# Optimization experiments

Measured on AMD Instinct MI355X. Metric: run time of the kernel, lower is better.

Reference implementation:

```python
import jax, jax.numpy as jnp
import numpy as np

IN_F, OUT_F, BLOCK, NBLK = 1024, 4096, 256, 16
TOPK = NBLK // 4  # 4, as in forward: n_blocks // 4


def setup_inputs() -> dict:
    key = jax.random.key(0)
    ks = jax.random.split(key, 7)
    s = 1.0 / np.sqrt(IN_F)
    s2 = 1.0 / np.sqrt(OUT_F)
    return {
        "x": jax.random.normal(ks[0], (4, 4096, IN_F), jnp.float32),
        "router_w": jax.random.uniform(ks[1], (NBLK, IN_F), jnp.float32, -s, s),
        "router_b": jax.random.uniform(ks[2], (NBLK,), jnp.float32, -s, s),
        "w1": jax.random.uniform(ks[3], (OUT_F, IN_F), jnp.float32, -s, s),
        "b1": jax.random.uniform(ks[4], (OUT_F,), jnp.float32, -s, s),
        "w2": jax.random.uniform(ks[5], (IN_F, OUT_F), jnp.float32, -s2, s2),
        "b2": jax.random.uniform(ks[6], (IN_F,), jnp.float32, -s2, s2),
    }


def reference(x, router_w, router_b, w1, b1, w2, b2):
    x_shape = x.shape
    xf = x.reshape(-1, IN_F)  # [N, d]
    n = xf.shape[0]
    # router: Linear + softmax, then top-k block selection per token
    prob = jax.nn.softmax(xf @ router_w.T + router_b, axis=-1)  # [N, n_blocks]
    _, idx = jax.lax.top_k(prob, TOPK)  # [N, k]
    mask = jnp.zeros((n, NBLK), bool).at[jnp.arange(n)[:, None], idx].set(True)
    # RoutedLinearRow: per-block fc1, zeros at unselected blocks
    w1b = w1.reshape(NBLK, BLOCK, IN_F)
    b1b = b1.reshape(NBLK, BLOCK)
    h = jnp.einsum('nd,ibd->nib', xf, w1b) + b1b  # [N, n_blocks, block]
    h = jnp.where(mask[:, :, None], h, jnp.zeros((), h.dtype))
    h = jax.nn.relu(h)
    # RoutedLinearCol: only selected blocks contribute
    w2b = w2.reshape(IN_F, NBLK, BLOCK)
    y = jnp.einsum('nib,dib->nd', jnp.where(mask[:, :, None], h, 0.0), w2b) + b2
    return y.reshape(x_shape)
```

## Files before the change

### kernel.cpp

```cpp
#include <hip/hip_runtime.h>
#include <hip/hip_bf16.h>

#define NTOK   16384
#define INF    1024
#define OUTF   4096
#define NBLK   16
#define BLKSZ  256
#define KTOP   4

typedef short bf16x8 __attribute__((ext_vector_type(8)));
typedef float f32x4 __attribute__((ext_vector_type(4)));
typedef unsigned short u16x8 __attribute__((ext_vector_type(8)));

__device__ __forceinline__ unsigned short f2bf(float f) {
  unsigned u = __float_as_uint(f);
  u += 0x7FFFu + ((u >> 16) & 1u);
  return (unsigned short)(u >> 16);
}

__device__ __forceinline__ void load_lds16(const void* g, void* l) {
  __builtin_amdgcn_global_load_lds(
      (const __attribute__((address_space(1))) unsigned int*)g,
      (__attribute__((address_space(3))) unsigned int*)l, 16, 0, 0);
}

__device__ __forceinline__ double shfl_xor_d(double v, int m) {
  long long l = __double_as_longlong(v);
  int lo = (int)(l & 0xFFFFFFFFll), hi = (int)(l >> 32);
  lo = __shfl_xor(lo, m);
  hi = __shfl_xor(hi, m);
  return __longlong_as_double(((long long)hi << 32) | (unsigned long long)(unsigned)lo);
}

__device__ __forceinline__ int pi_perm(int j) {
  return (j & 128) | ((j & 7) << 4) | ((j >> 3) & 15);
}

__global__ void k_zero(unsigned* __restrict__ list32, unsigned* __restrict__ counts) {
  int i = blockIdx.x * 256 + threadIdx.x;
  if (i < 33792) list32[i] = 0;
  else if (i < 33808) counts[i - 33792] = 0;
}

__global__ __launch_bounds__(256) void k_convert(
    const float* __restrict__ w1, const float* __restrict__ w2,
    const float* __restrict__ b1, unsigned short* __restrict__ w1b,
    unsigned short* __restrict__ w2p, float* __restrict__ b1p) {
  const size_t stride = (size_t)gridDim.x * 256;
  for (size_t i = (size_t)blockIdx.x * 256 + threadIdx.x; i < 1573376; i += stride) {
    if (i < 1048576) {
      float4 v = ((const float4*)w1)[i];
      ushort4 o;
      o.x = f2bf(v.x); o.y = f2bf(v.y); o.z = f2bf(v.z); o.w = f2bf(v.w);
      ((ushort4*)w1b)[i] = o;
    } else if (i < 1572864) {
      const size_t g = i - 1048576;
      const int d = (int)(g >> 9);
      const int rest = (int)(g & 511);
      const int jg = rest * 8;
      const int blk = jg >> 8;
      const int j0 = jg & 255;
      const float* src = w2 + (size_t)d * 4096 + blk * 256;
      u16x8 o;
#pragma unroll
      for (int ni = 0; ni < 8; ++ni) o[ni] = f2bf(src[pi_perm(j0 + ni)]);
      *(u16x8*)(w2p + (size_t)d * 4096 + jg) = o;
    } else {
      const int idx = (int)(i - 1572864);
      const int jg = idx * 8;
      const int blk = jg >> 8;
      const int j0 = jg & 255;
      const float* src = b1 + blk * 256;
      float o[8];
#pragma unroll
      for (int ni = 0; ni < 8; ++ni) o[ni] = src[pi_perm(j0 + ni)];
      float4* dst = (float4*)(b1p + jg);
      dst[0] = make_float4(o[0], o[1], o[2], o[3]);
      dst[1] = make_float4(o[4], o[5], o[6], o[7]);
    }
  }
}

__global__ __launch_bounds__(256) void k_router(
    const float* __restrict__ x, const float* __restrict__ rw,
    const float* __restrict__ rb, unsigned* __restrict__ tok_blocks,
    unsigned* __restrict__ counts, unsigned short* __restrict__ xb) {
  __shared__ float4 rwl[4096];
  const int tid = threadIdx.x;
  const float4* rw4 = (const float4*)rw;
  for (int i = tid; i < 4096; i += 256) rwl[i] = rw4[i];
  __syncthreads();

  const int n = blockIdx.x * 32 + (tid >> 3);
  const int q = tid & 7;
  double p[16];
#pragma unroll
  for (int j = 0; j < 16; ++j) p[j] = 0.0;
  const float4* xr = (const float4*)(x + (size_t)n * INF);
  ushort4* xbr = (ushort4*)(xb + (size_t)n * INF);
#pragma unroll 4
  for (int i = 0; i < 32; ++i) {
    const int d4 = q + i * 8;
    const float4 xv = xr[d4];
    ushort4 o;
    o.x = f2bf(xv.x); o.y = f2bf(xv.y); o.z = f2bf(xv.z); o.w = f2bf(xv.w);
    xbr[d4] = o;
#pragma unroll
    for (int j = 0; j < 16; ++j) {
      const float4 wv = rwl[j * 256 + d4];
      p[j] = fma((double)xv.x, (double)wv.x, p[j]);
      p[j] = fma((double)xv.y, (double)wv.y, p[j]);
      p[j] = fma((double)xv.z, (double)wv.z, p[j]);
      p[j] = fma((double)xv.w, (double)wv.w, p[j]);
    }
  }
#pragma unroll
  for (int j = 0; j < 16; ++j) {
    double v = p[j];
    v += shfl_xor_d(v, 1);
    v += shfl_xor_d(v, 2);
    v += shfl_xor_d(v, 4);
    p[j] = v + (double)rb[j];
  }

  __syncthreads();
  unsigned* hist = (unsigned*)rwl;
  if (tid < 16) hist[tid] = 0;
  __syncthreads();

  if (q == 0) {
    unsigned packed = 0;
#pragma unroll
    for (int j = 0; j < 16; ++j) {
      int r = 0;
#pragma unroll
      for (int j2 = 0; j2 < 16; ++j2)
        r += (int)((p[j2] > p[j]) | ((p[j2] == p[j]) & (j2 < j)));
      if (r < KTOP) packed |= (unsigned)j << (8 * r);
    }
    tok_blocks[n] = packed;
    atomicAdd(&hist[packed & 15u], 1u);
    atomicAdd(&hist[(packed >> 8) & 15u], 1u);
    atomicAdd(&hist[(packed >> 16) & 15u], 1u);
    atomicAdd(&hist[(packed >> 24) & 15u], 1u);
  }
  __syncthreads();
  if (tid < 16 && hist[tid]) atomicAdd(&counts[tid], hist[tid]);
}

__global__ void k_scan(const unsigned* __restrict__ counts, unsigned* __restrict__ off,
                       unsigned* __restrict__ cursors) {
  if (threadIdx.x == 0 && blockIdx.x == 0) {
    unsigned o = 0;
    for (int i = 0; i < 16; ++i) {
      off[i] = o; cursors[i] = o;
      o += (counts[i] + 127u) & ~127u;
    }
    off[16] = o;
  }
}

__global__ __launch_bounds__(256) void k_build(
    const unsigned* __restrict__ tok_blocks, unsigned* __restrict__ cursors,
    unsigned short* __restrict__ list, unsigned* __restrict__ inv) {
  const int n = blockIdx.x * 256 + threadIdx.x;
  const unsigned packed = tok_blocks[n];
  const int lane = threadIdx.x & 63;
  for (int b = 0; b < 16; ++b) {
    int r = -1;
#pragma unroll
    for (int q = 0; q < 4; ++q)
      if (((packed >> (8 * q)) & 15u) == (unsigned)b) r = q;
    unsigned long long m = __ballot(r >= 0);
    if (m) {
      int leader = __ffsll((unsigned long long)m) - 1;
      unsigned base = 0;
      if (lane == leader) base = atomicAdd(&cursors[b], (unsigned)__popcll(m));
      base = (unsigned)__shfl((int)base, leader);
      if (r >= 0) {
        unsigned pos = base + (unsigned)__popcll(m & ((1ull << lane) - 1ull));
        list[pos] = (unsigned short)n;
        inv[(size_t)n * 4 + r] = pos;
      }
    }
  }
}

__global__ __launch_bounds__(512, 1) void k_ffn(
    const unsigned short* __restrict__ xb, const unsigned short* __restrict__ w1b,
    const unsigned short* __restrict__ w2p, const float* __restrict__ b1p,
    const unsigned short* __restrict__ list, const unsigned* __restrict__ counts,
    const unsigned* __restrict__ off, unsigned short* __restrict__ part) {
  __shared__ __align__(16) char lds[114688];
  char* As  = lds + 65536;
  char* Bs  = lds + 81920;
  char* Bs2 = lds + 65536;
  __shared__ unsigned toks[128];

  const int bid0 = blockIdx.x;
  const int bid = (bid0 & 7) * 256 + (bid0 >> 3);
  const int blk = bid >> 7;
  const int tile = bid & 127;
  const unsigned cnt = counts[blk];
  if ((unsigned)(tile * 128) >= cnt) return;
  const unsigned goff = off[blk] + tile * 128;

  const int tid = threadIdx.x;
  const int lane = tid & 63;
  const int wid = tid >> 6;
  const int wr = wid >> 1;
  const int wc = wid & 1;
  const int asl = tid & 7;
  const int c16 = lane & 15;

  if (tid < 128) toks[tid] = list[goff + tid];
  __syncthreads();

  const unsigned tok0 = toks[tid >> 3];
  const unsigned tok1 = toks[64 + (tid >> 3)];

  f32x4 acc[2][8] = {};
  for (int k0 = 0; k0 < 1024; k0 += 64) {
    {
      const int row0 = tid >> 3;
      const int kcs0 = asl ^ (row0 & 7);
      load_lds16(xb + (size_t)tok0 * INF + k0 + kcs0 * 8, As + (wid * 64) * 16);
      const int row1 = 64 + row0;
      const int kcs1 = asl ^ (row1 & 7);
      load_lds16(xb + (size_t)tok1 * INF + k0 + kcs1 * 8, As + (512 + wid * 64) * 16);
    }
#pragma unroll
    for (int r = 0; r < 4; ++r) {
      const int row = (r * 512 + tid) >> 3;
      const int kcs = asl ^ (row & 7);
      load_lds16(w1b + ((size_t)(blk * 256 + row)) * INF + k0 + kcs * 8,
                 Bs + (r * 512 + wid * 64) * 16);
    }
    __syncthreads();
#pragma unroll
    for (int ks = 0; ks < 2; ++ks) {
      const int kc = ks * 4 + (lane >> 4);
      bf16x8 a[2], b[8];
#pragma unroll
      for (int mi = 0; mi < 2; ++mi) {
        const int row = wr * 32 + mi * 16 + (lane & 15);
        a[mi] = *(const bf16x8*)(As + row * 128 + ((kc ^ (row & 7)) << 4));
      }
#pragma unroll
      for (int ni = 0; ni < 8; ++ni) {
        const int row = wc * 128 + ni * 16 + (lane & 15);
        b[ni] = *(const bf16x8*)(Bs + row * 128 + ((kc ^ (row & 7)) << 4));
      }
#pragma unroll
      for (int mi = 0; mi < 2; ++mi)
#pragma unroll
        for (int ni = 0; ni < 8; ++ni)
          acc[mi][ni] = __builtin_amdgcn_mfma_f32_16x16x32_bf16(a[mi], b[ni], acc[mi][ni], 0, 0, 0);
    }
    __syncthreads();
  }

  {
    const float4* bp = (const float4*)(b1p + blk * 256 + wc * 128 + c16 * 8);
    const float4 bv0 = bp[0], bv1 = bp[1];
    const float bvv[8] = {bv0.x, bv0.y, bv0.z, bv0.w, bv1.x, bv1.y, bv1.z, bv1.w};
    const int chunk = wc * 16 + c16;
    const int cslot = (chunk & ~7);
    const int clow  = (chunk & 7);
#pragma unroll
    for (int mi = 0; mi < 2; ++mi) {
#pragma unroll
      for (int i = 0; i < 4; ++i) {
        const int row = wr * 32 + mi * 16 + (lane >> 4) * 4 + i;
        u16x8 wv;
#pragma unroll
        for (int ni = 0; ni < 8; ++ni) {
          float v = acc[mi][ni][i] + bvv[ni];
          v = v > 0.f ? v : 0.f;
          wv[ni] = f2bf(v);
        }
        *(u16x8*)(lds + row * 512 + ((cslot | (clow ^ (row & 7))) << 4)) = wv;
      }
    }
  }
  __syncthreads();

  for (int ns = 0; ns < 4; ++ns) {
    f32x4 acc2[2][8] = {};
    for (int k0 = 0; k0 < 256; k0 += 64) {
#pragma unroll
      for (int r = 0; r < 4; ++r) {
        const int row = (r * 512 + tid) >> 3;
        const int kcs = asl ^ (row & 7);
        load_lds16(w2p + (size_t)(ns * 256 + row) * OUTF + blk * 256 + k0 + kcs * 8,
                   Bs2 + (r * 512 + wid * 64) * 16);
      }
      __syncthreads();
#pragma unroll
      for (int ks = 0; ks < 2; ++ks) {
        const int kc = ks * 4 + (lane >> 4);
        bf16x8 a[2], b[8];
#pragma unroll
        for (int mi = 0; mi < 2; ++mi) {
          const int row = wr * 32 + mi * 16 + (lane & 15);
          a[mi] = *(const bf16x8*)(lds + row * 512 + k0 * 2 + ((kc ^ (row & 7)) << 4));
        }
#pragma unroll
        for (int ni = 0; ni < 8; ++ni) {
          const int row = wc * 128 + ni * 16 + (lane & 15);
          b[ni] = *(const bf16x8*)(Bs2 + row * 128 + ((kc ^ (row & 7)) << 4));
        }
#pragma unroll
        for (int mi = 0; mi < 2; ++mi)
#pragma unroll
          for (int ni = 0; ni < 8; ++ni)
            acc2[mi][ni] = __builtin_amdgcn_mfma_f32_16x16x32_bf16(a[mi], b[ni], acc2[mi][ni], 0, 0, 0);
      }
      __syncthreads();
    }
#pragma unroll
    for (int mi = 0; mi < 2; ++mi) {
#pragma unroll
      for (int i = 0; i < 4; ++i) {
        const int row = wr * 32 + mi * 16 + (lane >> 4) * 4 + i;
        u16x8 wv;
#pragma unroll
        for (int ni = 0; ni < 8; ++ni) wv[ni] = f2bf(acc2[mi][ni][i]);
        *(u16x8*)(part + (size_t)(goff + row) * 1024 + ns * 256 + wc * 128 + c16 * 8) = wv;
      }
    }
  }
}

__global__ __launch_bounds__(256) void k_reduce(const unsigned short* __restrict__ part,
                                                const unsigned* __restrict__ inv,
                                                const float* __restrict__ b2,
                                                float* __restrict__ out) {
  __shared__ float lds[8 * 1028];
  const int tid = threadIdx.x;
  const int tok0 = blockIdx.x * 8;
  const int tok_l = tid >> 5;
  const int l32 = tid & 31;

  const uint4 iv = *(const uint4*)(inv + (size_t)(tok0 + tok_l) * 4);
  const unsigned prow[4] = {iv.x, iv.y, iv.z, iv.w};

#pragma unroll
  for (int g = 0; g < 4; ++g) {
    const int idx = g * 32 + l32;
    const int p0 = idx * 8;
    float s[8] = {0.f, 0.f, 0.f, 0.f, 0.f, 0.f, 0.f, 0.f};
#pragma unroll
    for (int sl = 0; sl < 4; ++sl) {
      u16x8 v = *(const u16x8*)(part + (size_t)prow[sl] * 1024 + p0);
#pragma unroll
      for (int j = 0; j < 8; ++j)
        s[j] += __uint_as_float((unsigned)(unsigned short)v[j] << 16);
    }
    const int ns = idx >> 5, wcb = (idx >> 4) & 1, cc = idx & 15;
#pragma unroll
    for (int ni = 0; ni < 8; ++ni)
      lds[tok_l * 1028 + ns * 256 + wcb * 128 + ni * 16 + cc] = s[ni];
  }
  __syncthreads();
  const float4 b2v = ((const float4*)b2)[tid];
#pragma unroll
  for (int r = 0; r < 8; ++r) {
    f32x4 lv = *(f32x4*)&lds[r * 1028 + tid * 4];
    float4 o = make_float4(lv[0] + b2v.x, lv[1] + b2v.y, lv[2] + b2v.z, lv[3] + b2v.w);
    *(float4*)(out + (size_t)(tok0 + r) * 1024 + tid * 4) = o;
  }
}

extern "C" void kernel_launch(void* const* d_in, const int* in_sizes, int n_in,
                              void* d_out, int out_size, void* d_ws, size_t ws_size,
                              hipStream_t stream) {
  const float* x  = (const float*)d_in[0];
  const float* rw = (const float*)d_in[1];
  const float* rb = (const float*)d_in[2];
  const float* w1 = (const float*)d_in[3];
  const float* b1 = (const float*)d_in[4];
  const float* w2 = (const float*)d_in[5];
  const float* b2 = (const float*)d_in[6];
  float* out = (float*)d_out;

  char* ws = (char*)d_ws;
  unsigned short* part = (unsigned short*)(ws);
  unsigned short* xb   = (unsigned short*)(ws + 138412032);
  unsigned short* w1b  = (unsigned short*)(ws + 171966464);
  unsigned short* w2p  = (unsigned short*)(ws + 180355072);
  unsigned* tokb       = (unsigned*)(ws + 188743680);
  unsigned short* list = (unsigned short*)(ws + 188809216);
  unsigned* inv        = (unsigned*)(ws + 188944384);
  float* b1p           = (float*)(ws + 189206528);
  unsigned* counts     = (unsigned*)(ws + 189222912);
  unsigned* off        = (unsigned*)(ws + 189222976);
  unsigned* cursors    = (unsigned*)(ws + 189223104);

  k_zero<<<dim3(133), dim3(256), 0, stream>>>((unsigned*)list, counts);
  k_convert<<<dim3(1024), dim3(256), 0, stream>>>(w1, w2, b1, w1b, w2p, b1p);
  k_router<<<dim3(512), dim3(256), 0, stream>>>(x, rw, rb, tokb, counts, xb);
  k_scan<<<dim3(1), dim3(64), 0, stream>>>(counts, off, cursors);
  k_build<<<dim3(64), dim3(256), 0, stream>>>(tokb, cursors, list, inv);
  k_ffn<<<dim3(2048), dim3(512), 0, stream>>>(xb, w1b, w2p, b1p, list, counts, off, part);
  k_reduce<<<dim3(2048), dim3(256), 0, stream>>>(part, inv, b2, out);
}
```

Before: 292.5 us.

## Double-buffer LDS tiles in both FFN GEMM phases to overlap loads with MFMA

Enlarges shared memory to 160KB so each GEMM stage has two A/B buffers. The next k-tile's global-to-LDS loads are issued before the current tile's MFMA compute, in both the fc1 and fc2 loops. The first fc2 weight tile is prefetched during the bias/ReLU epilogue. Token indices are also read straight from global memory instead of being staged through LDS, which drops one barrier. The intent is to hide global load latency behind compute, at the cost of using the full LDS budget and more complex, macro-heavy control flow.

```diff
diff --git a/kernel.cpp b/kernel.cpp
--- a/kernel.cpp
+++ b/kernel.cpp
@@ -191,11 +191,11 @@
     const unsigned short* __restrict__ w2p, const float* __restrict__ b1p,
     const unsigned short* __restrict__ list, const unsigned* __restrict__ counts,
     const unsigned* __restrict__ off, unsigned short* __restrict__ part) {
-  __shared__ __align__(16) char lds[114688];
-  char* As  = lds + 65536;
-  char* Bs  = lds + 81920;
-  char* Bs2 = lds + 65536;
-  __shared__ unsigned toks[128];
+  __shared__ __align__(16) char lds[163840];
+  char* const As0 = lds + 65536;
+  char* const As1 = lds + 81920;
+  char* const Bs0 = lds + 98304;
+  char* const Bs1 = lds + 131072;
 
   const int bid0 = blockIdx.x;
   const int bid = (bid0 & 7) * 256 + (bid0 >> 3);
@@ -213,52 +213,107 @@
   const int asl = tid & 7;
   const int c16 = lane & 15;
 
-  if (tid < 128) toks[tid] = list[goff + tid];
-  __syncthreads();
-
-  const unsigned tok0 = toks[tid >> 3];
-  const unsigned tok1 = toks[64 + (tid >> 3)];
+  const unsigned tok0 = list[goff + (tid >> 3)];
+  const unsigned tok1 = list[goff + 64 + (tid >> 3)];
+  const int arow0 = tid >> 3;
+  const int arow1 = 64 + arow0;
+
+#define STAGE_A(buf, k0)                                                        \
+  {                                                                             \
+    load_lds16(xb + (size_t)tok0 * INF + (k0) + (asl ^ (arow0 & 7)) * 8,        \
+               (buf) + (wid * 64) * 16);                                        \
+    load_lds16(xb + (size_t)tok1 * INF + (k0) + (asl ^ (arow1 & 7)) * 8,        \
+               (buf) + (512 + wid * 64) * 16);                                  \
+  }
+
+#define STAGE_B1(buf, k0)                                                       \
+  _Pragma("unroll")                                                             \
+  for (int r = 0; r < 4; ++r) {                                                 \
+    const int row = (r * 512 + tid) >> 3;                                       \
+    load_lds16(w1b + ((size_t)(blk * 256 + row)) * INF + (k0) +                 \
+                   (asl ^ (row & 7)) * 8,                                       \
+               (buf) + (r * 512 + wid * 64) * 16);                              \
+  }
+
+#define COMPUTE_A(abuf, bbuf)                                                   \
+  _Pragma("unroll")                                                             \
+  for (int ks = 0; ks < 2; ++ks) {                                              \
+    const int kc = ks * 4 + (lane >> 4);                                        \
+    bf16x8 a[2], b[8];                                                          \
+    _Pragma("unroll")                                                           \
+    for (int mi = 0; mi < 2; ++mi) {                                            \
+      const int row = wr * 32 + mi * 16 + (lane & 15);                          \
+      a[mi] = *(const bf16x8*)((abuf) + row * 128 + ((kc ^ (row & 7)) << 4));   \
+    }                                                                           \
+    _Pragma("unroll")                                                           \
+    for (int ni = 0; ni < 8; ++ni) {                                            \
+      const int row = wc * 128 + ni * 16 + (lane & 15);                         \
+      b[ni] = *(const bf16x8*)((bbuf) + row * 128 + ((kc ^ (row & 7)) << 4));   \
+    }                                                                           \
+    _Pragma("unroll")                                                           \
+    for (int mi = 0; mi < 2; ++mi)                                              \
+      _Pragma("unroll")                                                         \
+      for (int ni = 0; ni < 8; ++ni)                                            \
+        acc[mi][ni] =                                                           \
+            __builtin_amdgcn_mfma_f32_16x16x32_bf16(a[mi], b[ni], acc[mi][ni], 0, 0, 0); \
+  }
 
   f32x4 acc[2][8] = {};
-  for (int k0 = 0; k0 < 1024; k0 += 64) {
-    {
-      const int row0 = tid >> 3;
-      const int kcs0 = asl ^ (row0 & 7);
-      load_lds16(xb + (size_t)tok0 * INF + k0 + kcs0 * 8, As + (wid * 64) * 16);
-      const int row1 = 64 + row0;
-      const int kcs1 = asl ^ (row1 & 7);
-      load_lds16(xb + (size_t)tok1 * INF + k0 + kcs1 * 8, As + (512 + wid * 64) * 16);
-    }
-#pragma unroll
-    for (int r = 0; r < 4; ++r) {
-      const int row = (r * 512 + tid) >> 3;
-      const int kcs = asl ^ (row & 7);
-      load_lds16(w1b + ((size_t)(blk * 256 + row)) * INF + k0 + kcs * 8,
-                 Bs + (r * 512 + wid * 64) * 16);
-    }
-    __syncthreads();
-#pragma unroll
-    for (int ks = 0; ks < 2; ++ks) {
-      const int kc = ks * 4 + (lane >> 4);
-      bf16x8 a[2], b[8];
-#pragma unroll
-      for (int mi = 0; mi < 2; ++mi) {
-        const int row = wr * 32 + mi * 16 + (lane & 15);
-        a[mi] = *(const bf16x8*)(As + row * 128 + ((kc ^ (row & 7)) << 4));
-      }
-#pragma unroll
-      for (int ni = 0; ni < 8; ++ni) {
-        const int row = wc * 128 + ni * 16 + (lane & 15);
-        b[ni] = *(const bf16x8*)(Bs + row * 128 + ((kc ^ (row & 7)) << 4));
-      }
-#pragma unroll
-      for (int mi = 0; mi < 2; ++mi)
-#pragma unroll
-        for (int ni = 0; ni < 8; ++ni)
-          acc[mi][ni] = __builtin_amdgcn_mfma_f32_16x16x32_bf16(a[mi], b[ni], acc[mi][ni], 0, 0, 0);
-    }
-    __syncthreads();
-  }
+  STAGE_A(As0, 0);
+  STAGE_B1(Bs0, 0);
+  __syncthreads();
+#pragma unroll 1
+  for (int kk = 0; kk < 8; ++kk) {
+    const int k0 = kk * 128;
+    STAGE_A(As1, k0 + 64);
+    STAGE_B1(Bs1, k0 + 64);
+    COMPUTE_A(As0, Bs0);
+    __syncthreads();
+    if (kk < 7) {
+      STAGE_A(As0, k0 + 128);
+      STAGE_B1(Bs0, k0 + 128);
+    }
+    COMPUTE_A(As1, Bs1);
+    __syncthreads();
+  }
+
+#define STAGE_B2(buf, it)                                                       \
+  {                                                                             \
+    const int ns2 = (it) >> 2, k02 = ((it) & 3) * 64;                           \
+    _Pragma("unroll")                                                           \
+    for (int r = 0; r < 4; ++r) {                                               \
+      const int row = (r * 512 + tid) >> 3;                                     \
+      load_lds16(w2p + (size_t)(ns2 * 256 + row) * OUTF + blk * 256 + k02 +     \
+                     (asl ^ (row & 7)) * 8,                                     \
+                 (buf) + (r * 512 + wid * 64) * 16);                            \
+    }                                                                           \
+  }
+
+#define COMPUTE_B(bbuf, k02)                                                    \
+  _Pragma("unroll")                                                             \
+  for (int ks = 0; ks < 2; ++ks) {                                              \
+    const int kc = ks * 4 + (lane >> 4);                                        \
+    bf16x8 a[2], b[8];                                                          \
+    _Pragma("unroll")                                                           \
+    for (int mi = 0; mi < 2; ++mi) {                                            \
+      const int row = wr * 32 + mi * 16 + (lane & 15);                          \
+      a[mi] = *(const bf16x8*)(lds + row * 512 + (k02) * 2 +                    \
+                               ((kc ^ (row & 7)) << 4));                        \
+    }                                                                           \
+    _Pragma("unroll")                                                           \
+    for (int ni = 0; ni < 8; ++ni) {                                            \
+      const int row = wc * 128 + ni * 16 + (lane & 15);                         \
+      b[ni] = *(const bf16x8*)((bbuf) + row * 128 + ((kc ^ (row & 7)) << 4));   \
+    }                                                                           \
+    _Pragma("unroll")                                                           \
+    for (int mi = 0; mi < 2; ++mi)                                              \
+      _Pragma("unroll")                                                         \
+      for (int ni = 0; ni < 8; ++ni)                                            \
+        acc2[mi][ni] =                                                          \
+            __builtin_amdgcn_mfma_f32_16x16x32_bf16(a[mi], b[ni], acc2[mi][ni], 0, 0, 0); \
+  }
+
+  STAGE_B2(Bs0, 0);
 
   {
     const float4* bp = (const float4*)(b1p + blk * 256 + wc * 128 + c16 * 8);
@@ -285,39 +340,22 @@
   }
   __syncthreads();
 
+#pragma unroll 1
   for (int ns = 0; ns < 4; ++ns) {
     f32x4 acc2[2][8] = {};
-    for (int k0 = 0; k0 < 256; k0 += 64) {
-#pragma unroll
-      for (int r = 0; r < 4; ++r) {
-        const int row = (r * 512 + tid) >> 3;
-        const int kcs = asl ^ (row & 7);
-        load_lds16(w2p + (size_t)(ns * 256 + row) * OUTF + blk * 256 + k0 + kcs * 8,
-                   Bs2 + (r * 512 + wid * 64) * 16);
-      }
-      __syncthreads();
-#pragma unroll
-      for (int ks = 0; ks < 2; ++ks) {
-        const int kc = ks * 4 + (lane >> 4);
-        bf16x8 a[2], b[8];
-#pragma unroll
-        for (int mi = 0; mi < 2; ++mi) {
-          const int row = wr * 32 + mi * 16 + (lane & 15);
-          a[mi] = *(const bf16x8*)(lds + row * 512 + k0 * 2 + ((kc ^ (row & 7)) << 4));
-        }
-#pragma unroll
-        for (int ni = 0; ni < 8; ++ni) {
-          const int row = wc * 128 + ni * 16 + (lane & 15);
-          b[ni] = *(const bf16x8*)(Bs2 + row * 128 + ((kc ^ (row & 7)) << 4));
-        }
-#pragma unroll
-        for (int mi = 0; mi < 2; ++mi)
-#pragma unroll
-          for (int ni = 0; ni < 8; ++ni)
-            acc2[mi][ni] = __builtin_amdgcn_mfma_f32_16x16x32_bf16(a[mi], b[ni], acc2[mi][ni], 0, 0, 0);
-      }
-      __syncthreads();
-    }
+    const int it0 = ns * 4;
+    STAGE_B2(Bs1, it0 + 1);
+    COMPUTE_B(Bs0, 0);
+    __syncthreads();
+    STAGE_B2(Bs0, it0 + 2);
+    COMPUTE_B(Bs1, 64);
+    __syncthreads();
+    STAGE_B2(Bs1, it0 + 3);
+    COMPUTE_B(Bs0, 128);
+    __syncthreads();
+    if (ns < 3) STAGE_B2(Bs0, it0 + 4);
+    COMPUTE_B(Bs1, 192);
+    __syncthreads();
 #pragma unroll
     for (int mi = 0; mi < 2; ++mi) {
 #pragma unroll
@@ -330,6 +368,11 @@
       }
     }
   }
+#undef STAGE_A
+#undef STAGE_B1
+#undef STAGE_B2
+#undef COMPUTE_A
+#undef COMPUTE_B
 }
 
 __global__ __launch_bounds__(256) void k_reduce(const unsigned short* __restrict__ part,
```

New measurement: 266.7 us. -8.8%, faster.
